# Kernel optimization log

Measured on AMD Instinct MI355X. Metric: run time of the kernel, lower is better.

## Reference

```python
import jax, jax.numpy as jnp
import numpy as np

RANK_W, SP_W, ANS_W = 1.0, 1.0, 1.0


def _listmle(thres, scores, labels):
    # thres [B,1], scores [B,P], labels [B,P] with values in {-1,0,1}
    fs = jnp.concatenate([thres, scores], axis=1)                      # [B,K]
    fl = jnp.concatenate([jnp.full_like(thres, 0.5), labels], axis=1)  # [B,K]
    s = jnp.exp(fs) * (fl != -1.0).astype(fs.dtype)
    # rest[b,j] = sum_k s[b,k] * (fl[b,k] < fl[b,j])  (sorting in the original
    # is only used to enumerate; with the 0.5 break it reduces to masking
    # entries with label >= 0.5)
    less = (fl[:, None, :] < fl[:, :, None]).astype(fs.dtype)          # [B,j,k]
    rest = jnp.einsum('bjk,bk->bj', less, s)
    mask = fl >= 0.5
    den = jnp.where(mask, s + rest, 1.0)
    logp = jnp.where(mask, fs - jnp.log(den), 0.0)  # log(s_j/(s_j+rest)) with s_j=exp(fs_j)
    return -jnp.sum(logp)


def setup_inputs() -> dict:
    key = jax.random.key(0)
    B, S, H, NS, NP, A = 8, 4096, 1024, 64, 32, 8
    ks = jax.random.split(key, 12)
    sequence_output = jax.random.normal(ks[0], (B, S, H), jnp.float32)
    token_type_ids = jax.random.randint(ks[1], (B, S), 0, 2).astype(jnp.int32)
    # strictly increasing sentence boundaries; last 4 sentences padded with -1
    base = jnp.round(jnp.linspace(8, S - 8, NS + 1)).astype(jnp.int32)
    sent_starts = jnp.broadcast_to(base, (B, NS + 1)).copy()
    sent_starts = sent_starts.at[:, -4:].set(-1)
    para_starts = jnp.sort(jax.random.randint(ks[2], (B, NP), 0, S), axis=1).astype(jnp.int32)
    para_labels = jax.random.randint(ks[3], (B, NP), -1, 2).astype(jnp.float32)
    sp_sent_labels = jax.random.randint(ks[4], (B, NS), -1, 2).astype(jnp.float32)
    starts = jax.random.randint(ks[5], (B, A), -1, S).astype(jnp.int32)
    ends = jax.random.randint(ks[6], (B, A), -1, S).astype(jnp.int32)
    Wqa = jax.random.normal(ks[7], (H, 2), jnp.float32) * 0.02
    bqa = jnp.zeros((2,), jnp.float32)
    Wrank = jax.random.normal(ks[8], (H, 1), jnp.float32) * 0.02
    brank = jnp.zeros((1,), jnp.float32)
    Wsp = jax.random.normal(ks[9], (H, 1), jnp.float32) * 0.02
    bsp = jnp.zeros((1,), jnp.float32)
    return {"sequence_output": sequence_output, "token_type_ids": token_type_ids,
            "sent_starts": sent_starts, "para_starts": para_starts,
            "para_labels": para_labels, "sp_sent_labels": sp_sent_labels,
            "starts": starts, "ends": ends, "Wqa": Wqa, "bqa": bqa,
            "Wrank": Wrank, "brank": brank, "Wsp": Wsp, "bsp": bsp}


def reference(sequence_output, token_type_ids, sent_starts, para_starts,
              para_labels, sp_sent_labels, starts, ends,
              Wqa, bqa, Wrank, brank, Wsp, bsp):
    B, S, H = sequence_output.shape
    logits = sequence_output @ Wqa + bqa                               # [B,S,2]
    tt1 = token_type_ids == 1
    start_logits = jnp.where(tt1, logits[..., 0], -jnp.inf)
    end_logits = jnp.where(tt1, logits[..., 1], -jnp.inf)

    rank_thres = sequence_output[:, 0, :] @ Wrank + brank              # [B,1]
    sent_thres = sequence_output[:, 0, :] @ Wsp + bsp                  # [B,1]

    # ragged per-sentence mean pooling via prefix sums
    csum = jnp.concatenate([jnp.zeros((B, 1, H), sequence_output.dtype),
                            jnp.cumsum(sequence_output, axis=1)], axis=1)  # [B,S+1,H]
    st = sent_starts[:, :-1]
    en = sent_starts[:, 1:]
    valid = en != -1                                                   # [B,NS]
    st_c = jnp.clip(st, 0, S)
    en_c = jnp.maximum(jnp.clip(en, 0, S), st_c + 1)
    NS = st.shape[1]
    g_en = jnp.take_along_axis(csum, jnp.broadcast_to(en_c[:, :, None], (B, NS, H)), axis=1)
    g_st = jnp.take_along_axis(csum, jnp.broadcast_to(st_c[:, :, None], (B, NS, H)), axis=1)
    seg_mean = (g_en - g_st) / (en_c - st_c)[:, :, None].astype(sequence_output.dtype)
    sent_rep = jnp.where(valid[:, :, None], seg_mean, sequence_output[:, -1:, :])
    sp_score = (sent_rep @ Wsp + bsp)[..., 0]                          # [B,NS]

    NP = para_starts.shape[1]
    para_rep = jnp.take_along_axis(
        sequence_output, jnp.broadcast_to(para_starts[:, :, None].astype(jnp.int32), (B, NP, H)), axis=1)
    para_score = (para_rep @ Wrank + brank)[..., 0]                    # [B,NP]

    rank_loss = _listmle(rank_thres, para_score, para_labels)
    sp_loss = _listmle(sent_thres, sp_score, sp_sent_labels)

    ls_start = jax.nn.log_softmax(start_logits, axis=-1)
    ls_end = jax.nn.log_softmax(end_logits, axis=-1)

    def ce(ls, tgt):  # CrossEntropy with ignore_index=-1, reduction='none'
        safe = jnp.clip(tgt, 0, S - 1)
        nll = -jnp.take_along_axis(ls, safe, axis=1)
        return jnp.where(tgt == -1, 0.0, nll)

    loss_tensor = ce(ls_start, starts) + ce(ls_end, ends)              # [B,A]
    lp = -loss_tensor
    lp = jnp.where(lp == 0.0, -jnp.inf, lp)
    m = jnp.sum(jnp.exp(lp), axis=1)                                   # [B]
    pos = m > 0
    span_loss = -jnp.sum(jnp.where(pos, jnp.log(jnp.where(pos, m, 1.0)), 0.0))

    loss = rank_loss * RANK_W + span_loss * ANS_W + sp_loss * SP_W
    return (loss, rank_loss * RANK_W, sp_loss * SP_W)
```

## Files before the change

kernel.cpp:

```cpp
#include <hip/hip_runtime.h>
#include <math.h>

#define B 8
#define S 4096
#define H 1024
#define NSEG 64
#define NPARA 32
#define NA 8
#define BS (B * S)
#define PAD(i) ((i) + ((i) >> 4))
#define ROWS_PER_BLK 16
#define BLKS_PER_B (S / ROWS_PER_BLK)
#define NBLK (B * BLKS_PER_B)

__device__ __forceinline__ float2 lse_merge(float2 A, float2 Bv)
{
    float m = fmaxf(A.x, Bv.x);
    float s = 0.f;
    if (A.y > 0.f)  s += A.y * expf(A.x - m);
    if (Bv.y > 0.f) s += Bv.y * expf(Bv.x - m);
    return make_float2(m, s);
}

__global__ __launch_bounds__(256) void dots_kernel(
    const float* __restrict__ seq,
    const float* __restrict__ Wqa,
    const float* __restrict__ Wsp,
    const float* __restrict__ Wrank,
    const int*   __restrict__ tt,
    float* __restrict__ scores,
    float4* __restrict__ lse_part,
    float* __restrict__ out)
{
    if (blockIdx.x == 0 && threadIdx.x == 0) {
        out[0] = 0.f; out[1] = 0.f; out[2] = 0.f;
    }
    const int blk   = blockIdx.x;
    const int b     = blk >> 8;
    const int rbase = (blk & 255) * ROWS_PER_BLK;
    const int w     = threadIdx.x >> 6;
    const int lane  = threadIdx.x & 63;

    __shared__ float  blkres[4][ROWS_PER_BLK];
    __shared__ float4 lsep[4];

    float wq0[4][4], wq1[4][4];
    float4 wspv[4], wrkv[4];
#pragma unroll
    for (int c = 0; c < 4; ++c) {
        int h0 = (lane + 64 * c) * 4;
#pragma unroll
        for (int j = 0; j < 4; ++j) {
            wq0[c][j] = Wqa[(h0 + j) * 2 + 0];
            wq1[c][j] = Wqa[(h0 + j) * 2 + 1];
        }
        wspv[c] = *(const float4*)(Wsp + h0);
        wrkv[c] = *(const float4*)(Wrank + h0);
    }

    const int* ttb = tt + b * S;
    float m0 = -INFINITY, s0 = 0.f, m1 = -INFINITY, s1 = 0.f;

    for (int i = 0; i < 4; ++i) {
        const int srow = rbase + w * 4 + i;
        const float4* row = (const float4*)(seq + ((size_t)b * S + srow) * H);
        float a0 = 0.f, a1 = 0.f, a2 = 0.f, a3 = 0.f;
#pragma unroll
        for (int c = 0; c < 4; ++c) {
            float4 v = row[lane + 64 * c];
            a0 += v.x * wq0[c][0] + v.y * wq0[c][1] + v.z * wq0[c][2] + v.w * wq0[c][3];
            a1 += v.x * wq1[c][0] + v.y * wq1[c][1] + v.z * wq1[c][2] + v.w * wq1[c][3];
            a2 += v.x * wspv[c].x + v.y * wspv[c].y + v.z * wspv[c].z + v.w * wspv[c].w;
            a3 += v.x * wrkv[c].x + v.y * wrkv[c].y + v.z * wrkv[c].z + v.w * wrkv[c].w;
        }
#pragma unroll
        for (int off = 32; off > 0; off >>= 1) {
            a0 += __shfl_xor(a0, off);
            a1 += __shfl_xor(a1, off);
            a2 += __shfl_xor(a2, off);
            a3 += __shfl_xor(a3, off);
        }
        if (ttb[srow] == 1) {
            float mn = fmaxf(m0, a0);
            s0 = s0 * expf(m0 - mn) + expf(a0 - mn); m0 = mn;
            mn = fmaxf(m1, a1);
            s1 = s1 * expf(m1 - mn) + expf(a1 - mn); m1 = mn;
        }
        if (lane == 0) {
            const int idx = w * 4 + i;
            blkres[0][idx] = a0; blkres[1][idx] = a1;
            blkres[2][idx] = a2; blkres[3][idx] = a3;
        }
    }
    if (lane == 0) lsep[w] = make_float4(m0, s0, m1, s1);
    __syncthreads();

    const int t = threadIdx.x;
    if (t < 64) {
        const int p = t >> 4, idx = t & 15;
        scores[p * BS + b * S + rbase + idx] = blkres[p][idx];
    }
    if (t == 0) {
        float2 L0 = make_float2(lsep[0].x, lsep[0].y);
        float2 L1 = make_float2(lsep[0].z, lsep[0].w);
#pragma unroll
        for (int i = 1; i < 4; ++i) {
            L0 = lse_merge(L0, make_float2(lsep[i].x, lsep[i].y));
            L1 = lse_merge(L1, make_float2(lsep[i].z, lsep[i].w));
        }
        lse_part[blk] = make_float4(L0.x, L0.y, L1.x, L1.y);
    }
}

__device__ __forceinline__ float blk_reduce1(float v, float* wred1, int t)
{
    const int lane = t & 63, w = t >> 6;
#pragma unroll
    for (int off = 32; off > 0; off >>= 1) v += __shfl_xor(v, off);
    if (lane == 0) wred1[w] = v;
    __syncthreads();
    float r = wred1[0] + wred1[1] + wred1[2] + wred1[3];
    __syncthreads();
    return r;
}

__device__ float listmle_block(const float* fs, const float* fl, float* se,
                               int n, float* wred1, int t)
{
    if (t < n) se[t] = (fl[t] != -1.0f) ? expf(fs[t]) : 0.0f;
    __syncthreads();
    float lp = 0.0f;
    if (t < n && fl[t] >= 0.5f) {
        float fj = fl[t];
        float rest = 0.0f;
        for (int k = 0; k < n; ++k)
            if (fl[k] < fj) rest += se[k];
        lp = fs[t] - logf(se[t] + rest);
    }
    float tot = blk_reduce1(lp, wred1, t);
    return -tot;
}

__global__ __launch_bounds__(256) void batch_kernel(
    const float*  __restrict__ scores,
    const float4* __restrict__ lse_part,
    const int*    __restrict__ tt,
    const int*    __restrict__ sent_starts,
    const int*    __restrict__ para_starts,
    const float*  __restrict__ para_labels,
    const float*  __restrict__ sp_labels,
    const int*    __restrict__ starts,
    const int*    __restrict__ ends,
    float* __restrict__ out)
{
    const int b = blockIdx.x;
    const int t = threadIdx.x;
    const int lane = t & 63, w = t >> 6;

    __shared__ float  a[PAD(S) + 1];
    __shared__ float4 lsew[4];
    __shared__ float  wred1[4];
    __shared__ float  fsb[1 + NSEG], flb[1 + NSEG], seb[1 + NSEG];
    __shared__ float  lse_sh[2];

    const float* p0 = scores + 0 * BS + b * S;
    const float* p1 = scores + 1 * BS + b * S;
    const float* p2 = scores + 2 * BS + b * S;
    const float* p3 = scores + 3 * BS + b * S;
    const int*   ttb = tt + b * S;

    {
        float4 P = lse_part[b * BLKS_PER_B + t];
        float2 L0 = make_float2(P.x, P.y);
        float2 L1 = make_float2(P.z, P.w);
#pragma unroll
        for (int off = 32; off > 0; off >>= 1) {
            float2 O0 = make_float2(__shfl_xor(L0.x, off), __shfl_xor(L0.y, off));
            float2 O1 = make_float2(__shfl_xor(L1.x, off), __shfl_xor(L1.y, off));
            L0 = lse_merge(L0, O0);
            L1 = lse_merge(L1, O1);
        }
        if (lane == 0) lsew[w] = make_float4(L0.x, L0.y, L1.x, L1.y);
        __syncthreads();
        if (t == 0) {
            float2 M0 = make_float2(lsew[0].x, lsew[0].y);
            float2 M1 = make_float2(lsew[0].z, lsew[0].w);
#pragma unroll
            for (int i = 1; i < 4; ++i) {
                M0 = lse_merge(M0, make_float2(lsew[i].x, lsew[i].y));
                M1 = lse_merge(M1, make_float2(lsew[i].z, lsew[i].w));
            }
            lse_sh[0] = M0.x + logf(M0.y);
            lse_sh[1] = M1.x + logf(M1.y);
        }
    }

    {
        for (int s = t; s < S; s += 256) a[PAD(s)] = p2[s];
        __syncthreads();
        float vals[16];
        float run = 0.f;
        const int base = t * 16;
#pragma unroll
        for (int i = 0; i < 16; ++i) {
            run += a[PAD(base + i)];
            vals[i] = run;
        }
        float v = run;
#pragma unroll
        for (int off = 1; off < 64; off <<= 1) {
            float u = __shfl_up(v, off, 64);
            if (lane >= off) v += u;
        }
        if (lane == 63) wred1[w] = v;
        __syncthreads();
        float woff = 0.f;
        for (int i = 0; i < w; ++i) woff += wred1[i];
        const float excl = woff + v - run;
        __syncthreads();
#pragma unroll
        for (int i = 0; i < 16; ++i) a[PAD(base + i + 1)] = excl + vals[i];
        if (t == 0) a[PAD(0)] = 0.f;
        __syncthreads();
    }

    if (t == 0) { fsb[0] = a[PAD(1)]; flb[0] = 0.5f; }
    if (t < NSEG) {
        int st = sent_starts[b * (NSEG + 1) + t];
        int en = sent_starts[b * (NSEG + 1) + t + 1];
        int stc = min(max(st, 0), S);
        int enc = max(min(max(en, 0), S), stc + 1);
        float score;
        if (en != -1) {
            int encc = min(enc, S);
            score = (a[PAD(encc)] - a[PAD(stc)]) / (float)(enc - stc);
        } else {
            score = a[PAD(S)] - a[PAD(S - 1)];
        }
        fsb[1 + t] = score;
        flb[1 + t] = sp_labels[b * NSEG + t];
    }
    __syncthreads();
    float sp_loss_b = listmle_block(fsb, flb, seb, 1 + NSEG, wred1, t);

    if (t == 0) { fsb[0] = p3[0]; flb[0] = 0.5f; }
    if (t < NPARA) {
        int ps = para_starts[b * NPARA + t];
        fsb[1 + t] = p3[ps];
        flb[1 + t] = para_labels[b * NPARA + t];
    }
    __syncthreads();
    float rank_loss_b = listmle_block(fsb, flb, seb, 1 + NPARA, wred1, t);

    float e_a = 0.f;
    if (t < NA) {
        const float lse0 = lse_sh[0], lse1 = lse_sh[1];
        int tsv = starts[b * NA + t];
        int tev = ends[b * NA + t];
        float lt = 0.f;
        if (tsv != -1) {
            int sf = min(max(tsv, 0), S - 1);
            float sl = (ttb[sf] == 1) ? p0[sf] : -INFINITY;
            lt += -(sl - lse0);
        }
        if (tev != -1) {
            int sf = min(max(tev, 0), S - 1);
            float el = (ttb[sf] == 1) ? p1[sf] : -INFINITY;
            lt += -(el - lse1);
        }
        float lp = -lt;
        e_a = (lp == 0.0f) ? 0.f : expf(lp);
    }
#pragma unroll
    for (int off = 4; off > 0; off >>= 1) e_a += __shfl_xor(e_a, off, 8);
    if (t == 0) {
        float logm = (e_a > 0.f) ? logf(e_a) : 0.f;
        atomicAdd(out + 0, rank_loss_b + sp_loss_b - logm);
        atomicAdd(out + 1, rank_loss_b);
        atomicAdd(out + 2, sp_loss_b);
    }
}

extern "C" void kernel_launch(void* const* d_in, const int* in_sizes, int n_in,
                              void* d_out, int out_size, void* d_ws, size_t ws_size,
                              hipStream_t stream)
{
    const float* seq         = (const float*)d_in[0];
    const int*   tt          = (const int*)  d_in[1];
    const int*   sent_starts = (const int*)  d_in[2];
    const int*   para_starts = (const int*)  d_in[3];
    const float* para_labels = (const float*)d_in[4];
    const float* sp_labels   = (const float*)d_in[5];
    const int*   starts      = (const int*)  d_in[6];
    const int*   ends        = (const int*)  d_in[7];
    const float* Wqa         = (const float*)d_in[8];
    const float* Wrank       = (const float*)d_in[10];
    const float* Wsp         = (const float*)d_in[12];

    float*  out      = (float*)d_out;
    float*  scores   = (float*)d_ws;
    float4* lse_part = (float4*)(scores + 4 * (size_t)BS);

    dots_kernel<<<NBLK, 256, 0, stream>>>(seq, Wqa, Wsp, Wrank, tt,
                                          scores, lse_part, out);
    batch_kernel<<<B, 256, 0, stream>>>(scores, lse_part, tt, sent_starts,
                                        para_starts, para_labels, sp_labels,
                                        starts, ends, out);
}
```

Before: 39.88 us.

## Double-buffer sequence rows into LDS via direct global-to-LDS loads

The dot-product kernel now stages each group of four rows into shared memory with global_load_lds, prefetching the next group while the current one is computed. Score outputs become interleaved float4 records (one per row) written directly, and the batch kernel reads the fields it needs from them. The intent is to hide memory latency on this bandwidth-bound pass and to make score stores coalesced. The cost is 32KB of LDS per block, which can lower occupancy, plus a barrier per group. A few edge-case reads in the batch kernel now come straight from global memory instead of the prefix array.

```diff
diff --git a/kernel.cpp b/kernel.cpp
--- a/kernel.cpp
+++ b/kernel.cpp
@@ -10,8 +10,16 @@
 #define BS (B * S)
 #define PAD(i) ((i) + ((i) >> 4))
 #define ROWS_PER_BLK 16
+#define GROUPS 4
 #define BLKS_PER_B (S / ROWS_PER_BLK)
 #define NBLK (B * BLKS_PER_B)
+
+__device__ __forceinline__ void gload_lds16(const float4* g, float4* l)
+{
+    __builtin_amdgcn_global_load_lds(
+        (const __attribute__((address_space(1))) void*)g,
+        (__attribute__((address_space(3))) void*)l, 16, 0, 0);
+}
 
 __device__ __forceinline__ float2 lse_merge(float2 A, float2 Bv)
 {
@@ -23,25 +31,24 @@
 }
 
 __global__ __launch_bounds__(256) void dots_kernel(
-    const float* __restrict__ seq,
-    const float* __restrict__ Wqa,
-    const float* __restrict__ Wsp,
-    const float* __restrict__ Wrank,
-    const int*   __restrict__ tt,
-    float* __restrict__ scores,
+    const float4* __restrict__ seq4,
+    const float*  __restrict__ Wqa,
+    const float*  __restrict__ Wsp,
+    const float*  __restrict__ Wrank,
+    const int*    __restrict__ tt,
+    float4* __restrict__ sc4,
     float4* __restrict__ lse_part,
-    float* __restrict__ out)
-{
-    if (blockIdx.x == 0 && threadIdx.x == 0) {
-        out[0] = 0.f; out[1] = 0.f; out[2] = 0.f;
-    }
+    float*  __restrict__ out)
+{
     const int blk   = blockIdx.x;
     const int b     = blk >> 8;
     const int rbase = (blk & 255) * ROWS_PER_BLK;
-    const int w     = threadIdx.x >> 6;
-    const int lane  = threadIdx.x & 63;
-
-    __shared__ float  blkres[4][ROWS_PER_BLK];
+    const int t     = threadIdx.x;
+    const int w     = t >> 6, lane = t & 63;
+
+    if (blk == 0 && t == 0) { out[0] = 0.f; out[1] = 0.f; out[2] = 0.f; }
+
+    __shared__ float4 sbuf[2][1024];
     __shared__ float4 lsep[4];
 
     float wq0[4][4], wq1[4][4];
@@ -58,16 +65,32 @@
         wrkv[c] = *(const float4*)(Wrank + h0);
     }
 
+    const size_t baseF4 = (size_t)(b * S + rbase) * (H / 4);
+    const int    wbase  = t & ~63;
+
+    {
+        const float4* gsrc = seq4 + baseF4;
+#pragma unroll
+        for (int k = 0; k < 4; ++k)
+            gload_lds16(gsrc + k * 256 + t, &sbuf[0][k * 256 + wbase]);
+    }
+    __syncthreads();
+
     const int* ttb = tt + b * S;
     float m0 = -INFINITY, s0 = 0.f, m1 = -INFINITY, s1 = 0.f;
 
-    for (int i = 0; i < 4; ++i) {
-        const int srow = rbase + w * 4 + i;
-        const float4* row = (const float4*)(seq + ((size_t)b * S + srow) * H);
+    for (int g = 0; g < GROUPS; ++g) {
+        if (g + 1 < GROUPS) {
+            const float4* gsrc = seq4 + baseF4 + (size_t)(g + 1) * (4 * H / 4);
+#pragma unroll
+            for (int k = 0; k < 4; ++k)
+                gload_lds16(gsrc + k * 256 + t, &sbuf[(g + 1) & 1][k * 256 + wbase]);
+        }
+        const float4* rowp = &sbuf[g & 1][w * 256];
         float a0 = 0.f, a1 = 0.f, a2 = 0.f, a3 = 0.f;
 #pragma unroll
         for (int c = 0; c < 4; ++c) {
-            float4 v = row[lane + 64 * c];
+            float4 v = rowp[lane + 64 * c];
             a0 += v.x * wq0[c][0] + v.y * wq0[c][1] + v.z * wq0[c][2] + v.w * wq0[c][3];
             a1 += v.x * wq1[c][0] + v.y * wq1[c][1] + v.z * wq1[c][2] + v.w * wq1[c][3];
             a2 += v.x * wspv[c].x + v.y * wspv[c].y + v.z * wspv[c].z + v.w * wspv[c].w;
@@ -80,26 +103,20 @@
             a2 += __shfl_xor(a2, off);
             a3 += __shfl_xor(a3, off);
         }
+        const int srow = rbase + g * 4 + w;
         if (ttb[srow] == 1) {
             float mn = fmaxf(m0, a0);
             s0 = s0 * expf(m0 - mn) + expf(a0 - mn); m0 = mn;
             mn = fmaxf(m1, a1);
             s1 = s1 * expf(m1 - mn) + expf(a1 - mn); m1 = mn;
         }
-        if (lane == 0) {
-            const int idx = w * 4 + i;
-            blkres[0][idx] = a0; blkres[1][idx] = a1;
-            blkres[2][idx] = a2; blkres[3][idx] = a3;
-        }
-    }
+        if (lane == 0)
+            sc4[b * S + srow] = make_float4(a0, a1, a2, a3);
+        __syncthreads();
+    }
+
     if (lane == 0) lsep[w] = make_float4(m0, s0, m1, s1);
     __syncthreads();
-
-    const int t = threadIdx.x;
-    if (t < 64) {
-        const int p = t >> 4, idx = t & 15;
-        scores[p * BS + b * S + rbase + idx] = blkres[p][idx];
-    }
     if (t == 0) {
         float2 L0 = make_float2(lsep[0].x, lsep[0].y);
         float2 L1 = make_float2(lsep[0].z, lsep[0].w);
@@ -142,7 +159,7 @@
 }
 
 __global__ __launch_bounds__(256) void batch_kernel(
-    const float*  __restrict__ scores,
+    const float4* __restrict__ sc4,
     const float4* __restrict__ lse_part,
     const int*    __restrict__ tt,
     const int*    __restrict__ sent_starts,
@@ -163,11 +180,8 @@
     __shared__ float  fsb[1 + NSEG], flb[1 + NSEG], seb[1 + NSEG];
     __shared__ float  lse_sh[2];
 
-    const float* p0 = scores + 0 * BS + b * S;
-    const float* p1 = scores + 1 * BS + b * S;
-    const float* p2 = scores + 2 * BS + b * S;
-    const float* p3 = scores + 3 * BS + b * S;
-    const int*   ttb = tt + b * S;
+    const float4* sb  = sc4 + (size_t)b * S;
+    const int*    ttb = tt + b * S;
 
     {
         float4 P = lse_part[b * BLKS_PER_B + t];
@@ -196,7 +210,7 @@
     }
 
     {
-        for (int s = t; s < S; s += 256) a[PAD(s)] = p2[s];
+        for (int s = t; s < S; s += 256) a[PAD(s)] = sb[s].z;
         __syncthreads();
         float vals[16];
         float run = 0.f;
@@ -224,7 +238,7 @@
         __syncthreads();
     }
 
-    if (t == 0) { fsb[0] = a[PAD(1)]; flb[0] = 0.5f; }
+    if (t == 0) { fsb[0] = sb[0].z; flb[0] = 0.5f; }
     if (t < NSEG) {
         int st = sent_starts[b * (NSEG + 1) + t];
         int en = sent_starts[b * (NSEG + 1) + t + 1];
@@ -235,7 +249,7 @@
             int encc = min(enc, S);
             score = (a[PAD(encc)] - a[PAD(stc)]) / (float)(enc - stc);
         } else {
-            score = a[PAD(S)] - a[PAD(S - 1)];
+            score = sb[S - 1].z;
         }
         fsb[1 + t] = score;
         flb[1 + t] = sp_labels[b * NSEG + t];
@@ -243,10 +257,10 @@
     __syncthreads();
     float sp_loss_b = listmle_block(fsb, flb, seb, 1 + NSEG, wred1, t);
 
-    if (t == 0) { fsb[0] = p3[0]; flb[0] = 0.5f; }
+    if (t == 0) { fsb[0] = sb[0].w; flb[0] = 0.5f; }
     if (t < NPARA) {
         int ps = para_starts[b * NPARA + t];
-        fsb[1 + t] = p3[ps];
+        fsb[1 + t] = sb[ps].w;
         flb[1 + t] = para_labels[b * NPARA + t];
     }
     __syncthreads();
@@ -260,12 +274,12 @@
         float lt = 0.f;
         if (tsv != -1) {
             int sf = min(max(tsv, 0), S - 1);
-            float sl = (ttb[sf] == 1) ? p0[sf] : -INFINITY;
+            float sl = (ttb[sf] == 1) ? sb[sf].x : -INFINITY;
             lt += -(sl - lse0);
         }
         if (tev != -1) {
             int sf = min(max(tev, 0), S - 1);
-            float el = (ttb[sf] == 1) ? p1[sf] : -INFINITY;
+            float el = (ttb[sf] == 1) ? sb[sf].y : -INFINITY;
             lt += -(el - lse1);
         }
         float lp = -lt;
@@ -298,12 +312,12 @@
     const float* Wsp         = (const float*)d_in[12];
 
     float*  out      = (float*)d_out;
-    float*  scores   = (float*)d_ws;
-    float4* lse_part = (float4*)(scores + 4 * (size_t)BS);
-
-    dots_kernel<<<NBLK, 256, 0, stream>>>(seq, Wqa, Wsp, Wrank, tt,
-                                          scores, lse_part, out);
-    batch_kernel<<<B, 256, 0, stream>>>(scores, lse_part, tt, sent_starts,
+    float4* sc4      = (float4*)d_ws;
+    float4* lse_part = sc4 + (size_t)BS;
+
+    dots_kernel<<<NBLK, 256, 0, stream>>>((const float4*)seq, Wqa, Wsp, Wrank,
+                                          tt, sc4, lse_part, out);
+    batch_kernel<<<B, 256, 0, stream>>>(sc4, lse_part, tt, sent_starts,
                                         para_starts, para_labels, sp_labels,
                                         starts, ends, out);
 }
```

Result: slower. 40.82 us (+2.3%).

## Replace block-wide prefix scan with direct per-segment sums by thread quads

Applied to the files above, without the earlier changes.

Removes the shared-memory prefix-sum over all 4096 sentence scores, which needed several block barriers. Each sentence segment is now summed directly from global memory by four cooperating threads combined with shuffles, and sentence starts are staged in shared memory. This removes the scan and the LDS staging, but each quad loops serially over its segment of about 64 elements with strided global loads. Summation order changes slightly, so float rounding can differ.

```diff
diff --git a/kernel.cpp b/kernel.cpp
--- a/kernel.cpp
+++ b/kernel.cpp
@@ -8,7 +8,6 @@
 #define NPARA 32
 #define NA 8
 #define BS (B * S)
-#define PAD(i) ((i) + ((i) >> 4))
 #define ROWS_PER_BLK 16
 #define BLKS_PER_B (S / ROWS_PER_BLK)
 #define NBLK (B * BLKS_PER_B)
@@ -157,17 +156,19 @@
     const int t = threadIdx.x;
     const int lane = t & 63, w = t >> 6;
 
-    __shared__ float  a[PAD(S) + 1];
     __shared__ float4 lsew[4];
     __shared__ float  wred1[4];
     __shared__ float  fsb[1 + NSEG], flb[1 + NSEG], seb[1 + NSEG];
     __shared__ float  lse_sh[2];
+    __shared__ int    ssh[NSEG + 1];
 
     const float* p0 = scores + 0 * BS + b * S;
     const float* p1 = scores + 1 * BS + b * S;
     const float* p2 = scores + 2 * BS + b * S;
     const float* p3 = scores + 3 * BS + b * S;
     const int*   ttb = tt + b * S;
+
+    if (t < NSEG + 1) ssh[t] = sent_starts[b * (NSEG + 1) + t];
 
     {
         float4 P = lse_part[b * BLKS_PER_B + t];
@@ -196,49 +197,28 @@
     }
 
     {
-        for (int s = t; s < S; s += 256) a[PAD(s)] = p2[s];
-        __syncthreads();
-        float vals[16];
-        float run = 0.f;
-        const int base = t * 16;
-#pragma unroll
-        for (int i = 0; i < 16; ++i) {
-            run += a[PAD(base + i)];
-            vals[i] = run;
-        }
-        float v = run;
-#pragma unroll
-        for (int off = 1; off < 64; off <<= 1) {
-            float u = __shfl_up(v, off, 64);
-            if (lane >= off) v += u;
-        }
-        if (lane == 63) wred1[w] = v;
-        __syncthreads();
-        float woff = 0.f;
-        for (int i = 0; i < w; ++i) woff += wred1[i];
-        const float excl = woff + v - run;
-        __syncthreads();
-#pragma unroll
-        for (int i = 0; i < 16; ++i) a[PAD(base + i + 1)] = excl + vals[i];
-        if (t == 0) a[PAD(0)] = 0.f;
-        __syncthreads();
-    }
-
-    if (t == 0) { fsb[0] = a[PAD(1)]; flb[0] = 0.5f; }
-    if (t < NSEG) {
-        int st = sent_starts[b * (NSEG + 1) + t];
-        int en = sent_starts[b * (NSEG + 1) + t + 1];
-        int stc = min(max(st, 0), S);
-        int enc = max(min(max(en, 0), S), stc + 1);
-        float score;
+        const int j  = t >> 2;
+        const int l4 = t & 3;
+        int st = ssh[j];
+        int en = ssh[j + 1];
         if (en != -1) {
-            int encc = min(enc, S);
-            score = (a[PAD(encc)] - a[PAD(stc)]) / (float)(enc - stc);
+            int stc = min(max(st, 0), S);
+            int enc = max(min(max(en, 0), S), stc + 1);
+            float x = 0.f;
+            for (int s = stc + l4; s < enc; s += 4) x += p2[s];
+            x += __shfl_xor(x, 1);
+            x += __shfl_xor(x, 2);
+            if (l4 == 0) {
+                fsb[1 + j] = x / (float)(enc - stc);
+                flb[1 + j] = sp_labels[b * NSEG + j];
+            }
         } else {
-            score = a[PAD(S)] - a[PAD(S - 1)];
-        }
-        fsb[1 + t] = score;
-        flb[1 + t] = sp_labels[b * NSEG + t];
+            if (l4 == 0) {
+                fsb[1 + j] = p2[S - 1];
+                flb[1 + j] = sp_labels[b * NSEG + j];
+            }
+        }
+        if (t == 0) { fsb[0] = p2[0]; flb[0] = 0.5f; }
     }
     __syncthreads();
     float sp_loss_b = listmle_block(fsb, flb, seb, 1 + NSEG, wred1, t);
```

Result: faster. 38.51 us (median of 2 runs) (-3.4%).
